# Kernel optimization log

Hardware: AMD Instinct MI355X
Metric: run time of the kernel (lower is better)

## Reference

```python
import jax, jax.numpy as jnp
import numpy as np

N_NODES = 50000
N_GRAPHS = 256
IN_DIM = 128
HID = 128
N_LAYERS = 3
N_EDGES = 800000


def setup_inputs() -> dict:
    key = jax.random.key(0)
    ks = jax.random.split(key, 16)
    x = jax.random.normal(ks[0], (N_NODES, IN_DIM), dtype=jnp.float32)
    edge_index = jax.random.randint(ks[1], (2, N_EDGES), 0, N_NODES, dtype=jnp.int64)
    batch = jnp.sort(jax.random.randint(ks[2], (N_NODES,), 0, N_GRAPHS, dtype=jnp.int64))
    inp = {"x": x, "edge_index": edge_index, "batch": batch}
    # SAGEConv params per PyG: lin_l (bias) applied to mean-aggregated neighbors,
    # lin_r (no bias) applied to the root node feature.
    dims = [(IN_DIM, HID)] + [(HID, HID)] * (N_LAYERS - 1)
    for i, (din, dout) in enumerate(dims):
        s = 1.0 / np.sqrt(din)
        inp[f"Wl{i}"] = jax.random.uniform(ks[3 + 3 * i], (din, dout), jnp.float32, -s, s)
        inp[f"bl{i}"] = jax.random.uniform(ks[4 + 3 * i], (dout,), jnp.float32, -s, s)
        inp[f"Wr{i}"] = jax.random.uniform(ks[5 + 3 * i], (din, dout), jnp.float32, -s, s)
    return inp


def _sage_conv(x, src, dst, Wl, bl, Wr):
    # mean aggregation of source-node messages into destination nodes
    msg = x[src]                                               # [E, d] gather
    agg = jax.ops.segment_sum(msg, dst, num_segments=N_NODES)  # [N, d] scatter-add
    deg = jax.ops.segment_sum(jnp.ones((src.shape[0], 1), x.dtype), dst,
                              num_segments=N_NODES)
    agg = agg / jnp.maximum(deg, 1.0)
    return agg @ Wl + bl + x @ Wr


def reference(x, edge_index, batch, Wl0, bl0, Wr0, Wl1, bl1, Wr1, Wl2, bl2, Wr2):
    src, dst = edge_index[0], edge_index[1]
    params = [(Wl0, bl0, Wr0), (Wl1, bl1, Wr1), (Wl2, bl2, Wr2)]
    h = x
    for Wl, bl, Wr in params:
        h = jax.nn.relu(_sage_conv(h, src, dst, Wl, bl, Wr))
        # dropout is a no-op in eval mode
    # meanmax readout over graph ids
    cnt = jax.ops.segment_sum(jnp.ones((h.shape[0], 1), h.dtype), batch,
                              num_segments=N_GRAPHS)
    g_mean = jax.ops.segment_sum(h, batch, num_segments=N_GRAPHS) / jnp.maximum(cnt, 1.0)
    g_max = jax.ops.segment_max(h, batch, num_segments=N_GRAPHS)
    g_max = jnp.where(jnp.isfinite(g_max), g_max, 0.0)  # empty graphs -> 0
    return jnp.concatenate([g_mean, g_max], axis=-1)    # [G, 2*HID]
```

## Files before the change

### kernel.cpp

```cpp
#include <hip/hip_runtime.h>
#include <hip/hip_bf16.h>
#include <stdint.h>

#define N_NODES  50000
#define N_GRAPHS 256
#define DIM      128
#define N_EDGES  800000
#define K2       256
#define N_STRIPS (N_NODES / 16)
#define PAD_CAP  64
#define NBUCKET  196
#define NCHUNK   256
#define CHUNK    3125

typedef __attribute__((ext_vector_type(8))) short  short8;
typedef __attribute__((ext_vector_type(4))) float  floatx4;

__device__ __forceinline__ ushort f2bf(float f) {
    union { float f; uint32_t u; } c; c.f = f;
    uint32_t u = c.u;
    return (ushort)((u + 0x7fffu + ((u >> 16) & 1u)) >> 16);
}
__device__ __forceinline__ float bf2f(ushort b) {
    union { uint32_t u; float f; } c; c.u = ((uint32_t)b) << 16;
    return c.f;
}

__global__ __launch_bounds__(256) void k_convert_x(const float* __restrict__ x,
                                                   ushort* __restrict__ xb) {
    int i = blockIdx.x * 256 + threadIdx.x;
    const int n4 = N_NODES * DIM / 4;
    if (i < n4) {
        float4 v = ((const float4*)x)[i];
        uint32_t lo = (uint32_t)f2bf(v.x) | ((uint32_t)f2bf(v.y) << 16);
        uint32_t hi = (uint32_t)f2bf(v.z) | ((uint32_t)f2bf(v.w) << 16);
        ((uint2*)xb)[i] = make_uint2(lo, hi);
    }
}

__global__ __launch_bounds__(256) void k_prep_w_all(const float* __restrict__ Wl0, const float* __restrict__ Wr0,
                                                    const float* __restrict__ Wl1, const float* __restrict__ Wr1,
                                                    const float* __restrict__ Wl2, const float* __restrict__ Wr2,
                                                    ushort* __restrict__ Wt) {
    int i = blockIdx.x * 256 + threadIdx.x;
    if (i < 3 * DIM * K2) {
        int layer = i / (DIM * K2);
        int j = i % (DIM * K2);
        int n = j / K2, k = j % K2;
        const float* Wl = (layer == 0) ? Wl0 : (layer == 1) ? Wl1 : Wl2;
        const float* Wr = (layer == 0) ? Wr0 : (layer == 1) ? Wr1 : Wr2;
        float v = (k < DIM) ? Wl[k * DIM + n] : Wr[(k - DIM) * DIM + n];
        Wt[i] = f2bf(v);
    }
}

__global__ __launch_bounds__(256) void k_hist(const int* __restrict__ dst,
                                              int* __restrict__ counts) {
    __shared__ int hist[NBUCKET];
    int t = threadIdx.x, b = blockIdx.x;
    if (t < NBUCKET) hist[t] = 0;
    __syncthreads();
    const int e0 = b * CHUNK;
    for (int i = t; i < CHUNK; i += 256)
        atomicAdd(&hist[dst[e0 + i] >> 8], 1);
    __syncthreads();
    if (t < NBUCKET) counts[b * NBUCKET + t] = hist[t];
}

__global__ __launch_bounds__(256) void k_scan_col(const int* __restrict__ counts,
                                                  int* __restrict__ off,
                                                  int* __restrict__ total) {
    __shared__ int buf[256];
    int t = threadIdx.x, j = blockIdx.x;
    int v = counts[t * NBUCKET + j];
    buf[t] = v;
    __syncthreads();
    #pragma unroll
    for (int d = 1; d < 256; d <<= 1) {
        int x = (t >= d) ? buf[t - d] : 0;
        __syncthreads();
        buf[t] += x;
        __syncthreads();
    }
    off[t * NBUCKET + j] = buf[t] - v;
    if (t == 255) total[j] = buf[255];
}

__global__ __launch_bounds__(256) void k_scan_total(const int* __restrict__ total,
                                                    int* __restrict__ basep) {
    __shared__ int buf[256];
    int t = threadIdx.x;
    int v = (t < NBUCKET) ? total[t] : 0;
    buf[t] = v;
    __syncthreads();
    #pragma unroll
    for (int d = 1; d < 256; d <<= 1) {
        int x = (t >= d) ? buf[t - d] : 0;
        __syncthreads();
        buf[t] += x;
        __syncthreads();
    }
    if (t < NBUCKET) basep[t] = buf[t] - v;
}

__global__ __launch_bounds__(256) void k_scatter(const int* __restrict__ src,
                                                 const int* __restrict__ dst,
                                                 const int* __restrict__ off,
                                                 const int* __restrict__ basep,
                                                 uint32_t* __restrict__ ebuf) {
    __shared__ int cur[NBUCKET];
    int t = threadIdx.x, b = blockIdx.x;
    if (t < NBUCKET) cur[t] = off[b * NBUCKET + t] + basep[t];
    __syncthreads();
    const int e0 = b * CHUNK;
    for (int i = t; i < CHUNK; i += 256) {
        int d = dst[e0 + i];
        int s = src[e0 + i];
        int p = atomicAdd(&cur[d >> 8], 1);
        ebuf[p] = ((uint32_t)(d & 255) << 16) | (uint32_t)s;
    }
}

__global__ __launch_bounds__(256) void k_build(const uint32_t* __restrict__ ebuf,
                                               const int* __restrict__ total,
                                               const int* __restrict__ basep,
                                               int* __restrict__ padded,
                                               int* __restrict__ cnt) {
    __shared__ int lcnt[256];
    int t = threadIdx.x, j = blockIdx.x;
    lcnt[t] = 0;
    __syncthreads();
    int b0 = basep[j], tot = total[j];
    for (int i = t; i < tot; i += 256) {
        uint32_t v = ebuf[b0 + i];
        int dl = (int)(v >> 16);
        int s  = (int)(v & 0xffffu);
        int p  = atomicAdd(&lcnt[dl], 1);
        if (p < PAD_CAP) padded[((size_t)j * 256 + dl) * PAD_CAP + p] = s;
    }
    __syncthreads();
    int node = j * 256 + t;
    if (node < N_NODES) cnt[node] = lcnt[t];
}

__global__ __launch_bounds__(256) void k_sort_adj(int* __restrict__ padded,
                                                  const int* __restrict__ cnt) {
    int wid  = threadIdx.x >> 6;
    int lane = threadIdx.x & 63;
    int node = blockIdx.x * 4 + wid;
    if (node >= N_NODES) return;
    int deg = cnt[node];
    int m   = deg < PAD_CAP ? deg : PAD_CAP;
    int* lst = padded + (size_t)node * PAD_CAP;
    int v = (lane < m) ? lst[lane] : 0x7fffffff;
    #pragma unroll
    for (int k = 2; k <= 64; k <<= 1) {
        #pragma unroll
        for (int j = k >> 1; j > 0; j >>= 1) {
            int other  = __shfl_xor(v, j, 64);
            bool down  = (lane & k) != 0;
            bool lower = (lane & j) == 0;
            v = (lower ^ down) ? min(v, other) : max(v, other);
        }
    }
    if (lane < m) lst[lane] = v;
}

__global__ __launch_bounds__(256) void k_gbounds(const int* __restrict__ batch,
                                                 int* __restrict__ gstart,
                                                 int* __restrict__ gend) {
    int i = blockIdx.x * 256 + threadIdx.x;
    if (i >= N_NODES) return;
    int g = batch[i];
    if (i == 0) gstart[g] = 0;
    int gn = (i + 1 < N_NODES) ? batch[i + 1] : -1;
    if (gn != g) {
        gend[g] = i + 1;
        if (gn >= 0) gstart[gn] = i + 1;
    }
}

template <bool OUT_F32>
__global__ __launch_bounds__(256) void k_layer(const ushort* __restrict__ h_in,
                                               const int* __restrict__ padded,
                                               const int* __restrict__ cnt,
                                               const ushort* __restrict__ Wt,
                                               const float* __restrict__ bias,
                                               ushort* __restrict__ out_bf,
                                               float* __restrict__ out_f) {
    __shared__ ushort sAgg[16 * DIM];
    int wid  = threadIdx.x >> 6;
    int lane = threadIdx.x & 63;
    int r0   = blockIdx.x * 16;
    const uint32_t* hw = (const uint32_t*)h_in;

    for (int q = 0; q < 4; ++q) {
        int node = r0 + wid * 4 + q;
        int deg = cnt[node];
        int m   = deg < PAD_CAP ? deg : PAD_CAP;
        const int* lst = padded + (size_t)node * PAD_CAP;
        float ax[4] = {0.f, 0.f, 0.f, 0.f};
        float ay[4] = {0.f, 0.f, 0.f, 0.f};
        for (int e = 0; e < m; e += 16) {
            int idx[16];
            uint32_t v[16];
            #pragma unroll
            for (int k = 0; k < 16; ++k) {
                int ek = e + k;
                idx[k] = lst[ek < m ? ek : m - 1];
            }
            #pragma unroll
            for (int k = 0; k < 16; ++k)
                v[k] = hw[(size_t)idx[k] * 64 + lane];
            #pragma unroll
            for (int k = 0; k < 16; ++k) {
                uint32_t w = (e + k < m) ? v[k] : 0u;
                ax[k & 3] += bf2f((ushort)(w & 0xffffu));
                ay[k & 3] += bf2f((ushort)(w >> 16));
            }
        }
        float axs = (ax[0] + ax[1]) + (ax[2] + ax[3]);
        float ays = (ay[0] + ay[1]) + (ay[2] + ay[3]);
        float inv = 1.0f / (float)(deg > 0 ? deg : 1);
        uint32_t o = (uint32_t)f2bf(axs * inv) | ((uint32_t)f2bf(ays * inv) << 16);
        ((uint32_t*)(sAgg + (wid * 4 + q) * DIM))[lane] = o;
    }
    __syncthreads();

    int row  = lane & 15;
    int quad = lane >> 4;
    short8 a[8];
    const ushort* srow = sAgg + row * DIM + quad * 8;
    #pragma unroll
    for (int ks = 0; ks < 4; ++ks) a[ks] = *(const short8*)(srow + ks * 32);
    const ushort* hrow = h_in + (size_t)(r0 + row) * DIM + quad * 8;
    #pragma unroll
    for (int ks = 0; ks < 4; ++ks) a[4 + ks] = *(const short8*)(hrow + ks * 32);

    #pragma unroll
    for (int c = 0; c < 2; ++c) {
        int ct  = wid * 2 + c;
        int col = ct * 16 + row;
        const ushort* wrow = Wt + (size_t)col * K2 + quad * 8;
        floatx4 acc = {0.f, 0.f, 0.f, 0.f};
        #pragma unroll
        for (int ks = 0; ks < 8; ++ks) {
            short8 b = *(const short8*)(wrow + ks * 32);
            acc = __builtin_amdgcn_mfma_f32_16x16x32_bf16(a[ks], b, acc, 0, 0, 0);
        }
        float bv = bias[col];
        #pragma unroll
        for (int r = 0; r < 4; ++r) {
            int m = r0 + quad * 4 + r;
            float v = acc[r] + bv;
            v = v > 0.f ? v : 0.f;
            if (OUT_F32) out_f[(size_t)m * DIM + col] = v;
            else         out_bf[(size_t)m * DIM + col] = f2bf(v);
        }
    }
}

__global__ __launch_bounds__(128) void k_readout(const float* __restrict__ h,
                                                 const int* __restrict__ batch,
                                                 float* __restrict__ out) {
    int d  = threadIdx.x;
    int n0 = blockIdx.x * 128;
    int n1 = min(n0 + 128, N_NODES);
    int cur = -1; float sum = 0.f, mx = 0.f;
    for (int i = n0; i < n1; ++i) {
        int g = batch[i];
        if (g != cur) {
            if (cur >= 0) {
                atomicAdd(&out[cur * 2 * DIM + d], sum);
                atomicMax((int*)&out[cur * 2 * DIM + DIM + d], __float_as_int(mx));
            }
            cur = g; sum = 0.f; mx = 0.f;
        }
        float v = h[(size_t)i * DIM + d];
        sum += v; mx = fmaxf(mx, v);
    }
    if (cur >= 0) {
        atomicAdd(&out[cur * 2 * DIM + d], sum);
        atomicMax((int*)&out[cur * 2 * DIM + DIM + d], __float_as_int(mx));
    }
}

__global__ __launch_bounds__(256) void k_finalize(float* __restrict__ out,
                                                  const int* __restrict__ gstart,
                                                  const int* __restrict__ gend) {
    int i = blockIdx.x * 256 + threadIdx.x;
    if (i < N_GRAPHS * DIM) {
        int g = i / DIM, d = i % DIM;
        int c = gend[g] - gstart[g];
        out[g * 2 * DIM + d] /= (float)(c > 0 ? c : 1);
    }
}

extern "C" void kernel_launch(void* const* d_in, const int* in_sizes, int n_in,
                              void* d_out, int out_size, void* d_ws, size_t ws_size,
                              hipStream_t stream) {
    const float* x     = (const float*)d_in[0];
    const int*   ei    = (const int*)d_in[1];
    const int*   src   = ei;
    const int*   dst   = ei + N_EDGES;
    const int*   batch = (const int*)d_in[2];
    const float* Wl[3] = {(const float*)d_in[3], (const float*)d_in[6], (const float*)d_in[9]};
    const float* bl[3] = {(const float*)d_in[4], (const float*)d_in[7], (const float*)d_in[10]};
    const float* Wr[3] = {(const float*)d_in[5], (const float*)d_in[8], (const float*)d_in[11]};
    float* out = (float*)d_out;

    char* base = (char*)d_ws;
    size_t o = 0;
    auto alloc = [&](size_t b) -> char* {
        char* p = base + o;
        o = (o + b + 255) & ~(size_t)255;
        return p;
    };
    int*     gstart = (int*)alloc((size_t)N_GRAPHS * 4);
    int*     gend   = (int*)alloc((size_t)N_GRAPHS * 4);
    size_t   zero_bytes = o;
    int*     cnt    = (int*)alloc((size_t)N_NODES * 4);
    int*     counts = (int*)alloc((size_t)NCHUNK * NBUCKET * 4);
    int*     offs   = (int*)alloc((size_t)NCHUNK * NBUCKET * 4);
    int*     total  = (int*)alloc((size_t)NBUCKET * 4);
    int*     basep  = (int*)alloc((size_t)NBUCKET * 4);
    uint32_t* ebuf  = (uint32_t*)alloc((size_t)N_EDGES * 4);
    int*     padded = (int*)alloc((size_t)N_NODES * PAD_CAP * 4);
    ushort*  xb     = (ushort*)alloc((size_t)N_NODES * DIM * 2);
    ushort*  ha     = (ushort*)alloc((size_t)N_NODES * DIM * 2);
    ushort*  hb     = (ushort*)alloc((size_t)N_NODES * DIM * 2);
    float*   h3     = (float*)alloc((size_t)N_NODES * DIM * 4);
    ushort*  Wt     = (ushort*)alloc((size_t)3 * DIM * K2 * 2);
    (void)ws_size; (void)n_in; (void)in_sizes;

    hipMemsetAsync(base, 0, zero_bytes, stream);
    hipMemsetAsync(d_out, 0, (size_t)out_size * 4, stream);

    k_convert_x<<<(N_NODES * DIM / 4 + 255) / 256, 256, 0, stream>>>(x, xb);
    k_prep_w_all<<<(3 * DIM * K2 + 255) / 256, 256, 0, stream>>>(
        Wl[0], Wr[0], Wl[1], Wr[1], Wl[2], Wr[2], Wt);

    k_hist<<<NCHUNK, 256, 0, stream>>>(dst, counts);
    k_scan_col<<<NBUCKET, 256, 0, stream>>>(counts, offs, total);
    k_scan_total<<<1, 256, 0, stream>>>(total, basep);
    k_scatter<<<NCHUNK, 256, 0, stream>>>(src, dst, offs, basep, ebuf);
    k_build<<<NBUCKET, 256, 0, stream>>>(ebuf, total, basep, padded, cnt);
    k_sort_adj<<<(N_NODES + 3) / 4, 256, 0, stream>>>(padded, cnt);
    k_gbounds<<<(N_NODES + 255) / 256, 256, 0, stream>>>(batch, gstart, gend);

    k_layer<false><<<N_STRIPS, 256, 0, stream>>>(xb, padded, cnt, Wt,              bl[0], ha, nullptr);
    k_layer<false><<<N_STRIPS, 256, 0, stream>>>(ha, padded, cnt, Wt + DIM * K2,   bl[1], hb, nullptr);
    k_layer<true ><<<N_STRIPS, 256, 0, stream>>>(hb, padded, cnt, Wt + 2 * DIM * K2, bl[2], nullptr, h3);

    k_readout<<<(N_NODES + 127) / 128, 128, 0, stream>>>(h3, batch, out);
    k_finalize<<<(N_GRAPHS * DIM + 255) / 256, 256, 0, stream>>>(out, gstart, gend);
}
```

Measured before the change: 365.1 us.

## Merge prep kernels and use 8-wave layer blocks with padded shared rows

Three small setup kernels (input conversion, weight transpose, graph bounds) are merged into one launch to cut launch overhead. The layer kernel now runs with 512 threads, so each wave aggregates two nodes instead of four and computes one 16-column MFMA tile instead of two. This raises parallelism for the latency-bound neighbour gather. Shared aggregation rows are padded to 136 elements to reduce LDS bank conflicts. The cost is more waves per block and higher per-block register and occupancy pressure.

```diff
diff --git a/kernel.cpp b/kernel.cpp
--- a/kernel.cpp
+++ b/kernel.cpp
@@ -12,6 +12,7 @@
 #define NBUCKET  196
 #define NCHUNK   256
 #define CHUNK    3125
+#define SROW     136
 
 typedef __attribute__((ext_vector_type(8))) short  short8;
 typedef __attribute__((ext_vector_type(4))) float  floatx4;
@@ -26,31 +27,49 @@
     return c.f;
 }
 
-__global__ __launch_bounds__(256) void k_convert_x(const float* __restrict__ x,
-                                                   ushort* __restrict__ xb) {
-    int i = blockIdx.x * 256 + threadIdx.x;
-    const int n4 = N_NODES * DIM / 4;
-    if (i < n4) {
-        float4 v = ((const float4*)x)[i];
-        uint32_t lo = (uint32_t)f2bf(v.x) | ((uint32_t)f2bf(v.y) << 16);
-        uint32_t hi = (uint32_t)f2bf(v.z) | ((uint32_t)f2bf(v.w) << 16);
-        ((uint2*)xb)[i] = make_uint2(lo, hi);
-    }
-}
-
-__global__ __launch_bounds__(256) void k_prep_w_all(const float* __restrict__ Wl0, const float* __restrict__ Wr0,
-                                                    const float* __restrict__ Wl1, const float* __restrict__ Wr1,
-                                                    const float* __restrict__ Wl2, const float* __restrict__ Wr2,
-                                                    ushort* __restrict__ Wt) {
-    int i = blockIdx.x * 256 + threadIdx.x;
-    if (i < 3 * DIM * K2) {
-        int layer = i / (DIM * K2);
-        int j = i % (DIM * K2);
-        int n = j / K2, k = j % K2;
-        const float* Wl = (layer == 0) ? Wl0 : (layer == 1) ? Wl1 : Wl2;
-        const float* Wr = (layer == 0) ? Wr0 : (layer == 1) ? Wr1 : Wr2;
-        float v = (k < DIM) ? Wl[k * DIM + n] : Wr[(k - DIM) * DIM + n];
-        Wt[i] = f2bf(v);
+__global__ __launch_bounds__(256) void k_prep(const float* __restrict__ x,
+                                              ushort* __restrict__ xb,
+                                              const float* __restrict__ Wl0, const float* __restrict__ Wr0,
+                                              const float* __restrict__ Wl1, const float* __restrict__ Wr1,
+                                              const float* __restrict__ Wl2, const float* __restrict__ Wr2,
+                                              ushort* __restrict__ Wt,
+                                              const int* __restrict__ batch,
+                                              int* __restrict__ gstart,
+                                              int* __restrict__ gend) {
+    const int CONV_BLOCKS = (N_NODES * DIM / 4 + 255) / 256;
+    const int W_BLOCKS    = (3 * DIM * K2 + 255) / 256;
+    int b = blockIdx.x;
+    if (b < CONV_BLOCKS) {
+        int i = b * 256 + threadIdx.x;
+        const int n4 = N_NODES * DIM / 4;
+        if (i < n4) {
+            float4 v = ((const float4*)x)[i];
+            uint32_t lo = (uint32_t)f2bf(v.x) | ((uint32_t)f2bf(v.y) << 16);
+            uint32_t hi = (uint32_t)f2bf(v.z) | ((uint32_t)f2bf(v.w) << 16);
+            ((uint2*)xb)[i] = make_uint2(lo, hi);
+        }
+    } else if (b < CONV_BLOCKS + W_BLOCKS) {
+        int i = (b - CONV_BLOCKS) * 256 + threadIdx.x;
+        if (i < 3 * DIM * K2) {
+            int layer = i / (DIM * K2);
+            int j = i % (DIM * K2);
+            int n = j / K2, k = j % K2;
+            const float* Wl = (layer == 0) ? Wl0 : (layer == 1) ? Wl1 : Wl2;
+            const float* Wr = (layer == 0) ? Wr0 : (layer == 1) ? Wr1 : Wr2;
+            float v = (k < DIM) ? Wl[k * DIM + n] : Wr[(k - DIM) * DIM + n];
+            Wt[i] = f2bf(v);
+        }
+    } else {
+        int i = (b - CONV_BLOCKS - W_BLOCKS) * 256 + threadIdx.x;
+        if (i < N_NODES) {
+            int g = batch[i];
+            if (i == 0) gstart[g] = 0;
+            int gn = (i + 1 < N_NODES) ? batch[i + 1] : -1;
+            if (gn != g) {
+                gend[g] = i + 1;
+                if (gn >= 0) gstart[gn] = i + 1;
+            }
+        }
     }
 }
 
@@ -166,36 +185,24 @@
     if (lane < m) lst[lane] = v;
 }
 
-__global__ __launch_bounds__(256) void k_gbounds(const int* __restrict__ batch,
-                                                 int* __restrict__ gstart,
-                                                 int* __restrict__ gend) {
-    int i = blockIdx.x * 256 + threadIdx.x;
-    if (i >= N_NODES) return;
-    int g = batch[i];
-    if (i == 0) gstart[g] = 0;
-    int gn = (i + 1 < N_NODES) ? batch[i + 1] : -1;
-    if (gn != g) {
-        gend[g] = i + 1;
-        if (gn >= 0) gstart[gn] = i + 1;
-    }
-}
-
 template <bool OUT_F32>
-__global__ __launch_bounds__(256) void k_layer(const ushort* __restrict__ h_in,
+__global__ __launch_bounds__(512) void k_layer(const ushort* __restrict__ h_in,
                                                const int* __restrict__ padded,
                                                const int* __restrict__ cnt,
                                                const ushort* __restrict__ Wt,
                                                const float* __restrict__ bias,
                                                ushort* __restrict__ out_bf,
                                                float* __restrict__ out_f) {
-    __shared__ ushort sAgg[16 * DIM];
+    __shared__ ushort sAgg[16 * SROW];
     int wid  = threadIdx.x >> 6;
     int lane = threadIdx.x & 63;
     int r0   = blockIdx.x * 16;
     const uint32_t* hw = (const uint32_t*)h_in;
 
-    for (int q = 0; q < 4; ++q) {
-        int node = r0 + wid * 4 + q;
+    #pragma unroll
+    for (int q = 0; q < 2; ++q) {
+        int slot = wid * 2 + q;
+        int node = r0 + slot;
         int deg = cnt[node];
         int m   = deg < PAD_CAP ? deg : PAD_CAP;
         const int* lst = padded + (size_t)node * PAD_CAP;
@@ -223,40 +230,36 @@
         float ays = (ay[0] + ay[1]) + (ay[2] + ay[3]);
         float inv = 1.0f / (float)(deg > 0 ? deg : 1);
         uint32_t o = (uint32_t)f2bf(axs * inv) | ((uint32_t)f2bf(ays * inv) << 16);
-        ((uint32_t*)(sAgg + (wid * 4 + q) * DIM))[lane] = o;
+        ((uint32_t*)(sAgg + slot * SROW))[lane] = o;
     }
     __syncthreads();
 
     int row  = lane & 15;
     int quad = lane >> 4;
     short8 a[8];
-    const ushort* srow = sAgg + row * DIM + quad * 8;
+    const ushort* srow = sAgg + row * SROW + quad * 8;
     #pragma unroll
     for (int ks = 0; ks < 4; ++ks) a[ks] = *(const short8*)(srow + ks * 32);
     const ushort* hrow = h_in + (size_t)(r0 + row) * DIM + quad * 8;
     #pragma unroll
     for (int ks = 0; ks < 4; ++ks) a[4 + ks] = *(const short8*)(hrow + ks * 32);
 
-    #pragma unroll
-    for (int c = 0; c < 2; ++c) {
-        int ct  = wid * 2 + c;
-        int col = ct * 16 + row;
-        const ushort* wrow = Wt + (size_t)col * K2 + quad * 8;
-        floatx4 acc = {0.f, 0.f, 0.f, 0.f};
-        #pragma unroll
-        for (int ks = 0; ks < 8; ++ks) {
-            short8 b = *(const short8*)(wrow + ks * 32);
-            acc = __builtin_amdgcn_mfma_f32_16x16x32_bf16(a[ks], b, acc, 0, 0, 0);
-        }
-        float bv = bias[col];
-        #pragma unroll
-        for (int r = 0; r < 4; ++r) {
-            int m = r0 + quad * 4 + r;
-            float v = acc[r] + bv;
-            v = v > 0.f ? v : 0.f;
-            if (OUT_F32) out_f[(size_t)m * DIM + col] = v;
-            else         out_bf[(size_t)m * DIM + col] = f2bf(v);
-        }
+    int col = wid * 16 + row;
+    const ushort* wrow = Wt + (size_t)col * K2 + quad * 8;
+    floatx4 acc2 = {0.f, 0.f, 0.f, 0.f};
+    #pragma unroll
+    for (int ks = 0; ks < 8; ++ks) {
+        short8 b = *(const short8*)(wrow + ks * 32);
+        acc2 = __builtin_amdgcn_mfma_f32_16x16x32_bf16(a[ks], b, acc2, 0, 0, 0);
+    }
+    float bv = bias[col];
+    #pragma unroll
+    for (int r = 0; r < 4; ++r) {
+        int mr = r0 + quad * 4 + r;
+        float v = acc2[r] + bv;
+        v = v > 0.f ? v : 0.f;
+        if (OUT_F32) out_f[(size_t)mr * DIM + col] = v;
+        else         out_bf[(size_t)mr * DIM + col] = f2bf(v);
     }
 }
 
@@ -336,9 +339,11 @@
     hipMemsetAsync(base, 0, zero_bytes, stream);
     hipMemsetAsync(d_out, 0, (size_t)out_size * 4, stream);
 
-    k_convert_x<<<(N_NODES * DIM / 4 + 255) / 256, 256, 0, stream>>>(x, xb);
-    k_prep_w_all<<<(3 * DIM * K2 + 255) / 256, 256, 0, stream>>>(
-        Wl[0], Wr[0], Wl[1], Wr[1], Wl[2], Wr[2], Wt);
+    const int CONV_BLOCKS = (N_NODES * DIM / 4 + 255) / 256;
+    const int W_BLOCKS    = (3 * DIM * K2 + 255) / 256;
+    const int GB_BLOCKS   = (N_NODES + 255) / 256;
+    k_prep<<<CONV_BLOCKS + W_BLOCKS + GB_BLOCKS, 256, 0, stream>>>(
+        x, xb, Wl[0], Wr[0], Wl[1], Wr[1], Wl[2], Wr[2], Wt, batch, gstart, gend);
 
     k_hist<<<NCHUNK, 256, 0, stream>>>(dst, counts);
     k_scan_col<<<NBUCKET, 256, 0, stream>>>(counts, offs, total);
@@ -346,11 +351,10 @@
     k_scatter<<<NCHUNK, 256, 0, stream>>>(src, dst, offs, basep, ebuf);
     k_build<<<NBUCKET, 256, 0, stream>>>(ebuf, total, basep, padded, cnt);
     k_sort_adj<<<(N_NODES + 3) / 4, 256, 0, stream>>>(padded, cnt);
-    k_gbounds<<<(N_NODES + 255) / 256, 256, 0, stream>>>(batch, gstart, gend);
-
-    k_layer<false><<<N_STRIPS, 256, 0, stream>>>(xb, padded, cnt, Wt,              bl[0], ha, nullptr);
-    k_layer<false><<<N_STRIPS, 256, 0, stream>>>(ha, padded, cnt, Wt + DIM * K2,   bl[1], hb, nullptr);
-    k_layer<true ><<<N_STRIPS, 256, 0, stream>>>(hb, padded, cnt, Wt + 2 * DIM * K2, bl[2], nullptr, h3);
+
+    k_layer<false><<<N_STRIPS, 512, 0, stream>>>(xb, padded, cnt, Wt,                bl[0], ha, nullptr);
+    k_layer<false><<<N_STRIPS, 512, 0, stream>>>(ha, padded, cnt, Wt + DIM * K2,     bl[1], hb, nullptr);
+    k_layer<true ><<<N_STRIPS, 512, 0, stream>>>(hb, padded, cnt, Wt + 2 * DIM * K2, bl[2], nullptr, h3);
 
     k_readout<<<(N_NODES + 127) / 128, 128, 0, stream>>>(h3, batch, out);
     k_finalize<<<(N_GRAPHS * DIM + 255) / 256, 256, 0, stream>>>(out, gstart, gend);
```

New measurement: 397.7 us. 1.09x slower.
